# Kernel optimization log

Hardware: AMD Instinct MI355X
Metric: run time of the kernel (lower is better)

## Reference

```python
import jax, jax.numpy as jnp
import numpy as np

B, S, D, E, N = 2, 1024, 1024, 64, 16  # batch, seq, model_dim, embedding_dim, num_splats


def setup_inputs() -> dict:
    key = jax.random.key(0)
    ks = jax.random.split(key, 8)
    inv_sqrt_d = 1.0 / np.sqrt(D)
    return {
        "token_embeddings": jax.random.normal(ks[0], (B, S, D), jnp.float32),
        # position encoder Linear(D, E)
        "pos_W": jax.random.normal(ks[1], (D, E), jnp.float32) * inv_sqrt_d,
        "pos_b": jnp.zeros((E,), jnp.float32),
        "positional_bias": jax.random.normal(ks[2], (1024, E), jnp.float32) * 0.01,
        "splat_positions": jax.random.normal(ks[3], (N, E), jnp.float32) * 0.2,
        "splat_log_scales": jnp.zeros((N,), jnp.float32),
        # q/k/v Linear(D, D, bias=False)
        "q_W": jax.random.normal(ks[4], (D, D), jnp.float32) * inv_sqrt_d,
        "k_W": jax.random.normal(ks[5], (D, D), jnp.float32) * inv_sqrt_d,
        "v_W": jax.random.normal(ks[6], (D, D), jnp.float32) * inv_sqrt_d,
        "splat_gates": jnp.full((N,), 0.5, jnp.float32),
        "residual_weight": jnp.asarray(0.8, jnp.float32),
        "ln_w": jnp.ones((D,), jnp.float32),
        "ln_b": jnp.zeros((D,), jnp.float32),
    }


def reference(token_embeddings, pos_W, pos_b, positional_bias, splat_positions,
              splat_log_scales, q_W, k_W, v_W, splat_gates, residual_weight,
              ln_w, ln_b):
    b, s, d = token_embeddings.shape
    # token positions in splat embedding space: tanh(Linear(x)) + pos_bias[:S]
    positions = jnp.tanh(token_embeddings @ pos_W + pos_b) + positional_bias[:s][None]  # [B,S,E]
    # spatial influence per splat: Gaussian of distance, clamped scales, floor 0.01
    diff = positions[:, :, None, :] - splat_positions[None, None]  # [B,S,N,E]
    dist_sq = jnp.sum(diff * diff, axis=-1)                         # [B,S,N]
    scales = jnp.clip(jnp.exp(splat_log_scales), 0.3, 2.0)
    influence = jnp.maximum(jnp.exp(-0.5 * dist_sq / (scales * scales)), 0.01)  # [B,S,N]

    q = token_embeddings @ q_W
    k = token_embeddings @ k_W
    v = token_embeddings @ v_W

    w = jnp.transpose(influence, (2, 0, 1))      # [N,B,S]
    qw = q[None] * w[..., None]                  # [N,B,S,D]
    kw = k[None] * w[..., None]
    scores = jnp.einsum('nbid,nbjd->nbij', qw, kw) / jnp.sqrt(jnp.asarray(d, jnp.float32))
    causal = jnp.tril(jnp.ones((s, s), bool))
    scores = jnp.where(causal[None, None], scores, -1e9)
    attn = jax.nn.softmax(scores, axis=-1)       # [N,B,S,S]
    out = jnp.einsum('nbij,bjd->nbid', attn, v)  # [N,B,S,D]

    gates = jax.nn.sigmoid(splat_gates)[:, None, None, None]
    combined = jnp.mean(out * gates, axis=0)     # [B,S,D]

    rw = jax.nn.sigmoid(residual_weight)
    o = rw * token_embeddings + (1.0 - rw) * combined
    # LayerNorm (eps=1e-5)
    mu = jnp.mean(o, axis=-1, keepdims=True)
    var = jnp.mean((o - mu) ** 2, axis=-1, keepdims=True)
    return (o - mu) / jnp.sqrt(var + 1e-5) * ln_w + ln_b
```

## Files before the change

### kernel.cpp

```cpp
#include <hip/hip_runtime.h>
#include <hip/hip_bf16.h>
#include <hip/hip_fp16.h>

using bf16 = __hip_bfloat16;
typedef __attribute__((ext_vector_type(8))) short short8;
typedef __attribute__((ext_vector_type(4))) float f32x4;

static constexpr int Bb = 2, Ss = 1024, Dd = 1024, Ee = 64, Nn = 16;

struct Params {
    const float *X, *posW, *posB, *pbias, *spos, *lsc, *qW, *kW, *vW, *gates, *rwp, *lnw, *lnb;
    bf16 *Xb, *Wt, *WpT, *QKV, *Vt, *Aav;
    __half *wh;
    float *qk, *cb, *out;
};

__device__ __forceinline__ unsigned short f2bfr(float f) {
    __hip_bfloat16 h = __float2bfloat16(f);
    return *reinterpret_cast<unsigned short*>(&h);
}

#define GL_LDS(gp, lp) __builtin_amdgcn_global_load_lds( \
    (const __attribute__((address_space(1))) void*)(gp), \
    (__attribute__((address_space(3))) void*)(lp), 16, 0, 0)

__device__ __forceinline__ void do_transpose_f2b(
    const float* __restrict__ in, bf16* __restrict__ out,
    int R, int C, int bx, int by, char* sm)
{
    float (*tile)[65] = (float(*)[65])sm;
    int tx = threadIdx.x & 63, ty = threadIdx.x >> 6;
    int r0 = by * 64, c0 = bx * 64;
    #pragma unroll
    for (int i = 0; i < 16; ++i)
        tile[ty + i*4][tx] = in[(long)(r0 + ty + i*4)*C + c0 + tx];
    __syncthreads();
    #pragma unroll
    for (int i = 0; i < 16; ++i)
        out[(long)(c0 + ty + i*4)*R + r0 + tx] = __float2bfloat16(tile[tx][ty + i*4]);
    __syncthreads();
}

__device__ __forceinline__ void do_gemm6464(
    const bf16* __restrict__ Ab, const bf16* __restrict__ Bw, float* __restrict__ C,
    int Nc, int m0, int n0, int kBeg, int kEnd, float scale, char* sm)
{
    int tid = threadIdx.x, wid = tid >> 6, lane = tid & 63;
    int r16 = lane & 15, quad = lane >> 4;

    f32x4 acc[4];
    #pragma unroll
    for (int j = 0; j < 4; ++j)
        #pragma unroll
        for (int c = 0; c < 4; ++c) acc[j][c] = 0.f;

    const short* Ag = (const short*)Ab;
    const short* Bg = (const short*)Bw;

    int row2[2], kg2[2];
    #pragma unroll
    for (int j = 0; j < 2; ++j) {
        int c = tid + j*256; row2[j] = c >> 3; kg2[j] = (c & 7) ^ (row2[j] & 7);
    }

    auto stage = [&](int k0, int cr) {
        short* sA = (short*)(sm + cr*16384);
        short* sB = (short*)(sm + cr*16384 + 8192);
        #pragma unroll
        for (int j = 0; j < 2; ++j) {
            GL_LDS(Ag + (long)(m0 + row2[j])*1024 + k0 + kg2[j]*8, sA + (tid + j*256)*8);
            GL_LDS(Bg + (long)(n0 + row2[j])*1024 + k0 + kg2[j]*8, sB + (tid + j*256)*8);
        }
    };

    stage(kBeg, 0);
    __syncthreads();
    int cur = 0;
    for (int k0 = kBeg; k0 < kEnd; k0 += 64) {
        if (k0 + 64 < kEnd) stage(k0 + 64, cur ^ 1);
        short* lA = (short*)(sm + cur*16384);
        short* lB = (short*)(sm + cur*16384 + 8192);
        #pragma unroll
        for (int kk = 0; kk < 2; ++kk) {
            int kc = kk*4 + quad;
            int ra = wid*16 + r16;
            short8 af = *(const short8*)(lA + ra*64 + (kc ^ (ra & 7))*8);
            #pragma unroll
            for (int j = 0; j < 4; ++j) {
                int rb = j*16 + r16;
                short8 bfv = *(const short8*)(lB + rb*64 + (kc ^ (rb & 7))*8);
                acc[j] = __builtin_amdgcn_mfma_f32_16x16x32_bf16(af, bfv, acc[j], 0, 0, 0);
            }
        }
        __syncthreads();
        cur ^= 1;
    }

    #pragma unroll
    for (int j = 0; j < 4; ++j)
        #pragma unroll
        for (int rr = 0; rr < 4; ++rr)
            C[(long)(m0 + wid*16 + quad*4 + rr)*Nc + n0 + j*16 + r16] =
                acc[j][rr] * scale;
}

template<int OUT_MODE>
__device__ __forceinline__ void do_gemm128(
    const bf16* __restrict__ Ab, const bf16* __restrict__ Bw, void* __restrict__ Cv,
    int Nc, int m0, int n0, char* sm)
{
    int tid = threadIdx.x, wid = tid >> 6, lane = tid & 63;
    int wm = (wid >> 1) * 64, wnn = (wid & 1) * 64;
    int r16 = lane & 15, quad = lane >> 4;

    f32x4 acc[4][4];
    #pragma unroll
    for (int i = 0; i < 4; ++i)
        #pragma unroll
        for (int j = 0; j < 4; ++j)
            #pragma unroll
            for (int c = 0; c < 4; ++c) acc[i][j][c] = 0.f;

    const short* Ag = (const short*)Ab;
    const short* Bg = (const short*)Bw;

    int rowc[4], kgc[4];
    #pragma unroll
    for (int j = 0; j < 4; ++j) {
        int c = tid + j*256; rowc[j] = c >> 3; kgc[j] = (c & 7) ^ (rowc[j] & 7);
    }

    auto stage = [&](int k0, int cr) {
        short* sA = (short*)(sm + cr*32768);
        short* sB = (short*)(sm + cr*32768 + 16384);
        #pragma unroll
        for (int j = 0; j < 4; ++j)
            GL_LDS(Ag + (long)(m0 + rowc[j])*1024 + k0 + kgc[j]*8, sA + (tid + j*256)*8);
        #pragma unroll
        for (int j = 0; j < 4; ++j)
            GL_LDS(Bg + (long)(n0 + rowc[j])*1024 + k0 + kgc[j]*8, sB + (tid + j*256)*8);
    };

    stage(0, 0);
    __syncthreads();
    int cur = 0;
    for (int k0 = 0; k0 < 1024; k0 += 64) {
        if (k0 + 64 < 1024) stage(k0 + 64, cur ^ 1);
        short* lA = (short*)(sm + cur*32768);
        short* lB = (short*)(sm + cur*32768 + 16384);
        #pragma unroll
        for (int kk = 0; kk < 2; ++kk) {
            int kc = kk*4 + quad;
            short8 af[4], bfv[4];
            #pragma unroll
            for (int i = 0; i < 4; ++i) {
                int r = wm + i*16 + r16;
                af[i] = *(const short8*)(lA + r*64 + (kc ^ (r & 7))*8);
            }
            #pragma unroll
            for (int j = 0; j < 4; ++j) {
                int r = wnn + j*16 + r16;
                bfv[j] = *(const short8*)(lB + r*64 + (kc ^ (r & 7))*8);
            }
            #pragma unroll
            for (int i = 0; i < 4; ++i)
                #pragma unroll
                for (int j = 0; j < 4; ++j)
                    acc[i][j] = __builtin_amdgcn_mfma_f32_16x16x32_bf16(af[i], bfv[j], acc[i][j], 0, 0, 0);
        }
        __syncthreads();
        cur ^= 1;
    }

    if (OUT_MODE == 1) {
        bf16* C = (bf16*)Cv;
        #pragma unroll
        for (int i = 0; i < 4; ++i)
            #pragma unroll
            for (int j = 0; j < 4; ++j)
                #pragma unroll
                for (int rr = 0; rr < 4; ++rr)
                    C[(long)(m0 + wm + i*16 + quad*4 + rr)*Nc + n0 + wnn + j*16 + r16] =
                        __float2bfloat16(acc[i][j][rr]);
    } else {
        __syncthreads();
        bf16 (*lt)[132] = (bf16(*)[132])sm;
        #pragma unroll
        for (int i = 0; i < 4; ++i)
            #pragma unroll
            for (int j = 0; j < 4; ++j)
                #pragma unroll
                for (int rr = 0; rr < 4; ++rr)
                    lt[wnn + j*16 + r16][wm + i*16 + quad*4 + rr] =
                        __float2bfloat16(acc[i][j][rr]);
        __syncthreads();
        bf16* Vb = (bf16*)Cv + (long)(m0 >> 10) * Dd * Ss;
        int s0 = m0 & (Ss - 1);
        int colBase = wid * 32 + (lane >> 4);
        int idx = (lane & 15) * 8;
        #pragma unroll
        for (int it = 0; it < 8; ++it) {
            int col = colBase + it * 4;
            ushort4 v0 = *(const ushort4*)&lt[col][idx];
            ushort4 v1 = *(const ushort4*)&lt[col][idx + 4];
            *(ushort4*)(Vb + (long)(n0 + col)*Ss + s0 + idx)     = v0;
            *(ushort4*)(Vb + (long)(n0 + col)*Ss + s0 + idx + 4) = v1;
        }
    }
}

__device__ __forceinline__ void do_pos(const Params& p, int m0, char* sm)
{
    float (*P)[65]  = (float(*)[65])(sm + 16384);
    float (*sp)[65] = (float(*)[65])(sm + 16384 + 64*65*4);

    int tid = threadIdx.x, wid = tid >> 6, lane = tid & 63;
    int r16 = lane & 15, quad = lane >> 4;

    for (int idx = tid; idx < 16*64; idx += 256)
        sp[idx >> 6][idx & 63] = p.spos[idx];

    f32x4 acc[4];
    #pragma unroll
    for (int j = 0; j < 4; ++j)
        #pragma unroll
        for (int c = 0; c < 4; ++c) acc[j][c] = 0.f;

    int ra = tid >> 2, ka = (tid & 3) * 8;
    const short* Ag = (const short*)p.Xb;
    const short* Bg = (const short*)p.WpT;

    auto stage = [&](int k0, int cr) {
        short* sA = (short*)(sm + cr*8192);
        short* sB = (short*)(sm + cr*8192 + 4096);
        GL_LDS(Ag + (long)(m0+ra)*1024 + k0 + ka, sA + tid*8);
        GL_LDS(Bg + (long)ra*1024 + k0 + ka,      sB + tid*8);
    };

    stage(0, 0);
    __syncthreads();
    int cur = 0;
    for (int k0 = 0; k0 < Dd; k0 += 32) {
        if (k0 + 32 < Dd) stage(k0 + 32, cur ^ 1);
        short* lA = (short*)(sm + cur*8192);
        short* lB = (short*)(sm + cur*8192 + 4096);
        short8 af = *(const short8*)(lA + (wid*16 + r16)*32 + quad*8);
        #pragma unroll
        for (int j = 0; j < 4; ++j) {
            short8 bfv = *(const short8*)(lB + (j*16 + r16)*32 + quad*8);
            acc[j] = __builtin_amdgcn_mfma_f32_16x16x32_bf16(af, bfv, acc[j], 0, 0, 0);
        }
        __syncthreads();
        cur ^= 1;
    }

    #pragma unroll
    for (int j = 0; j < 4; ++j)
        #pragma unroll
        for (int rr = 0; rr < 4; ++rr) {
            int rl  = wid*16 + quad*4 + rr;
            int col = j*16 + r16;
            int srow = (m0 + rl) & (Ss - 1);
            P[rl][col] = tanhf(acc[j][rr] + p.posB[col]) + p.pbias[srow*Ee + col];
        }
    __syncthreads();

    int n  = tid & 15;
    int rb = (tid >> 4) * 4;
    float sc = __expf(p.lsc[n]);
    sc = fminf(fmaxf(sc, 0.3f), 2.0f);
    float inv2 = -0.5f / (sc * sc);
    #pragma unroll
    for (int rr = 0; rr < 4; ++rr) {
        int row = rb + rr;
        float d2 = 0.f;
        #pragma unroll 16
        for (int e = 0; e < 64; ++e) {
            float df = P[row][e] - sp[n][e];
            d2 += df * df;
        }
        float infl = fmaxf(__expf(d2 * inv2), 0.01f);
        p.wh[(long)(m0 + row)*Nn + n] = __float2half(infl);
    }
}

__global__ __launch_bounds__(256) void k_prep(Params p)
{
    __shared__ __align__(16) char sm[64*65*4];
    int z = blockIdx.z;
    if (z < 3) {
        const float* w = (z == 0) ? p.qW : (z == 1) ? p.kW : p.vW;
        do_transpose_f2b(w, p.Wt + (long)z*Dd*Dd, Dd, Dd, blockIdx.x, blockIdx.y, sm);
    } else if (blockIdx.x == 0) {
        do_transpose_f2b(p.posW, p.WpT, Dd, Ee, 0, blockIdx.y, sm);
    } else {
        int job = blockIdx.y * 15 + (blockIdx.x - 1);
        const float4* src = (const float4*)p.X;
        ushort4* dst = (ushort4*)p.Xb;
        for (int idx = job*256 + (int)threadIdx.x; idx < Bb*Ss*Dd/4; idx += 240*256) {
            float4 v = src[idx];
            ushort4 y;
            y.x = f2bfr(v.x); y.y = f2bfr(v.y); y.z = f2bfr(v.z); y.w = f2bfr(v.w);
            dst[idx] = y;
        }
    }
}

__global__ __launch_bounds__(256) void k_qkv_pos(Params p)
{
    __shared__ __align__(16) char sm[65536];
    int job = blockIdx.x;
    if (job < 384) {
        int z = job >> 7, t = job & 127;
        int bm = t >> 3, bn = t & 7;
        if (z < 2)
            do_gemm128<1>(p.Xb, p.Wt + (long)z*Dd*Dd, p.QKV + (long)z*2048*1024,
                          Dd, bm*128, bn*128, sm);
        else
            do_gemm128<2>(p.Xb, p.Wt + (long)2*Dd*Dd, p.Vt,
                          Dd, bm*128, bn*128, sm);
    } else {
        do_pos(p, (job - 384)*64, sm);
    }
}

__global__ __launch_bounds__(256) void k_qkt(Params p)
{
    __shared__ __align__(16) char sm[32768];
    int job = blockIdx.x;
    int b = job / 136, t = job % 136;
    int acc = 0, bm = 0, bn = 0;
    #pragma unroll
    for (int u = 0; u < 16; ++u) {
        int c = u + 1;
        if (t < acc + c) { bm = u; bn = t - acc; break; }
        acc += c;
    }
    const bf16* Qb = p.QKV + (long)b*Ss*Dd;
    const bf16* Kb = p.QKV + (long)2048*1024 + (long)b*Ss*Dd;
    float* dst = p.qk + (long)b*Ss*Ss;
    do_gemm6464(Qb, Kb, dst, Ss, bm*64, bn*64, 0, 1024, 0.03125f, sm);
}

__global__ __launch_bounds__(256) void k_softmax(Params p)
{
    __shared__ __align__(16) char sm[36864 + 256 + 16384];
    __half2 (*wt)[9] = (__half2(*)[9])sm;
    float (*wi4)[16] = (float(*)[16])(sm + 36864);
    float (*qc)[Ss]  = (float(*)[Ss])(sm + 36864 + 256);

    int base = blockIdx.x * 4, b = blockIdx.y;
    int tid = threadIdx.x, wid = tid >> 6, lane = tid & 63;
    int imax = base + 3;

    const __half*  whb  = p.wh + (long)b*Ss*Nn;
    const __half2* whb2 = (const __half2*)whb;

    for (int j = tid; j <= imax; j += 256) {
        #pragma unroll
        for (int h = 0; h < 8; ++h)
            wt[j][h] = whb2[j*8 + h];
    }
    if (tid < 64) wi4[tid >> 4][tid & 15] =
        __half2float(whb[(long)(base + (tid >> 4))*16 + (tid & 15)]);
    __syncthreads();

    int i = base + wid;
    long roff = ((long)b*Ss + i)*Ss;
    const float* q0 = p.qk + roff;
    bf16* arow      = p.Aav + roff;

    float wiR[16], l[16];
    #pragma unroll
    for (int n = 0; n < 16; ++n) { wiR[n] = wi4[wid][n]; l[n] = 0.f; }

    for (int j = lane; j <= i; j += 64) {
        float q = q0[j];
        qc[wid][j] = q;
        #pragma unroll
        for (int h = 0; h < 8; ++h) {
            float2 f = __half22float2(wt[j][h]);
            l[2*h]     += __expf(wiR[2*h]     * f.x * q);
            l[2*h + 1] += __expf(wiR[2*h + 1] * f.y * q);
        }
    }
    #pragma unroll
    for (int n = 0; n < 16; ++n)
        #pragma unroll
        for (int off = 32; off > 0; off >>= 1)
            l[n] += __shfl_xor(l[n], off);

    float coef[16];
    #pragma unroll
    for (int n = 0; n < 16; ++n) {
        float g  = p.gates[n];
        float sg = 1.f / (1.f + __expf(-g));
        coef[n]  = sg / (16.f * l[n]);
    }

    int jLim = (i | 63) + 1;
    for (int j = lane; j < jLim; j += 64) {
        float a = 0.f;
        if (j <= i) {
            float q = qc[wid][j];
            #pragma unroll
            for (int h = 0; h < 8; ++h) {
                float2 f = __half22float2(wt[j][h]);
                a += coef[2*h]     * __expf(wiR[2*h]     * f.x * q);
                a += coef[2*h + 1] * __expf(wiR[2*h + 1] * f.y * q);
            }
        }
        arow[j] = __float2bfloat16(a);
    }
}

__global__ __launch_bounds__(256) void k_av(Params p)
{
    __shared__ __align__(16) char sm[32768];
    int job = blockIdx.x;
    int b  = job >> 8;
    int r  = job & 255;
    int bm = 15 - (r >> 4);
    int bn = r & 15;
    int kEnd = (bm + 1) * 64;

    const bf16* Ab = p.Aav + (long)b*Ss*Ss;
    const bf16* Bw = p.Vt + (long)b*Dd*Ss;
    float* dst = p.cb + (long)b*Ss*Dd;
    do_gemm6464(Ab, Bw, dst, Dd, bm*64, bn*64, 0, kEnd, 1.f, sm);
}

__global__ __launch_bounds__(256) void k_epilogue(Params p)
{
    __shared__ float rs[4], rq[4];
    long row = blockIdx.x;
    int tid = threadIdx.x, wid = tid >> 6, lane = tid & 63;
    float rw = 1.f / (1.f + __expf(-p.rwp[0]));

    float4 c  = ((const float4*)(p.cb + row*Dd))[tid];
    float4 xv = ((const float4*)(p.X + row*Dd))[tid];

    float o[4];
    o[0] = rw * xv.x + (1.f - rw) * c.x;
    o[1] = rw * xv.y + (1.f - rw) * c.y;
    o[2] = rw * xv.z + (1.f - rw) * c.z;
    o[3] = rw * xv.w + (1.f - rw) * c.w;

    float sm1 = o[0] + o[1] + o[2] + o[3];
    float sq  = o[0]*o[0] + o[1]*o[1] + o[2]*o[2] + o[3]*o[3];
    #pragma unroll
    for (int off = 32; off > 0; off >>= 1) { sm1 += __shfl_xor(sm1, off); sq += __shfl_xor(sq, off); }
    if (lane == 0) { rs[wid] = sm1; rq[wid] = sq; }
    __syncthreads();
    sm1 = rs[0] + rs[1] + rs[2] + rs[3];
    sq  = rq[0] + rq[1] + rq[2] + rq[3];
    float mu  = sm1 * (1.f/1024.f);
    float var = sq * (1.f/1024.f) - mu*mu;
    float inv = rsqrtf(var + 1e-5f);

    float4 lw = ((const float4*)p.lnw)[tid];
    float4 lb = ((const float4*)p.lnb)[tid];
    float4 y;
    y.x = (o[0] - mu)*inv*lw.x + lb.x;
    y.y = (o[1] - mu)*inv*lw.y + lb.y;
    y.z = (o[2] - mu)*inv*lw.z + lb.z;
    y.w = (o[3] - mu)*inv*lw.w + lb.w;
    ((float4*)(p.out + row*Dd))[tid] = y;
}

extern "C" void kernel_launch(void* const* d_in, const int* in_sizes, int n_in,
                              void* d_out, int out_size, void* d_ws, size_t ws_size,
                              hipStream_t stream)
{
    Params prm;
    prm.X     = (const float*)d_in[0];
    prm.posW  = (const float*)d_in[1];
    prm.posB  = (const float*)d_in[2];
    prm.pbias = (const float*)d_in[3];
    prm.spos  = (const float*)d_in[4];
    prm.lsc   = (const float*)d_in[5];
    prm.qW    = (const float*)d_in[6];
    prm.kW    = (const float*)d_in[7];
    prm.vW    = (const float*)d_in[8];
    prm.gates = (const float*)d_in[9];
    prm.rwp   = (const float*)d_in[10];
    prm.lnw   = (const float*)d_in[11];
    prm.lnb   = (const float*)d_in[12];

    char* ws = (char*)d_ws;
    size_t off = 0;
    prm.Xb  = (bf16*)(ws + off);   off += (size_t)Bb*Ss*Dd*2;
    prm.Wt  = (bf16*)(ws + off);   off += (size_t)3*Dd*Dd*2;
    prm.WpT = (bf16*)(ws + off);   off += (size_t)Ee*Dd*2;
    prm.QKV = (bf16*)(ws + off);   off += (size_t)2*2048*1024*2;
    prm.Vt  = (bf16*)(ws + off);   off += (size_t)Bb*Dd*Ss*2;
    prm.Aav = (bf16*)(ws + off);   off += (size_t)Bb*Ss*Ss*2;
    prm.wh  = (__half*)(ws + off); off += (size_t)Bb*Ss*Nn*2;
    prm.qk  = (float*)(ws + off);  off += (size_t)Bb*Ss*Ss*4;
    prm.cb  = (float*)(ws + off);  off += (size_t)Bb*Ss*Dd*4;
    prm.out = (float*)d_out;
    (void)ws_size;

    k_prep    <<<dim3(16,16,4), 256, 0, stream>>>(prm);
    k_qkv_pos <<<416,            256, 0, stream>>>(prm);
    k_qkt     <<<272,            256, 0, stream>>>(prm);
    k_softmax <<<dim3(256, 2),   256, 0, stream>>>(prm);
    k_av      <<<512,            256, 0, stream>>>(prm);
    k_epilogue<<<2048,           256, 0, stream>>>(prm);
}
```

Before: 165.2 us.

## Shrink QKV GEMM tiles to 64x128, stage outputs through LDS, reorder pos jobs

The QKV projection GEMM now uses 64x128 tiles instead of 128x128, raising the block count from 384 to 768 so the 256 CUs get a fuller first wave. Output writes now go through LDS and are stored as 16-byte vector rows, replacing scattered 2-byte stores. The position-encoder blocks are moved to the front of the grid so they are scheduled first. Smaller tiles lower data reuse per block and add more global loads of the A operand, plus an extra LDS round trip in the epilogue.

After: 165.1 us. No clear change (-0.0%).

```diff
diff --git a/kernel.cpp b/kernel.cpp
--- a/kernel.cpp
+++ b/kernel.cpp
@@ -104,41 +104,44 @@
                 acc[j][rr] * scale;
 }
 
-template<int OUT_MODE>
-__device__ __forceinline__ void do_gemm128(
+template<int OUT>
+__device__ __forceinline__ void do_gemm64x128(
     const bf16* __restrict__ Ab, const bf16* __restrict__ Bw, void* __restrict__ Cv,
     int Nc, int m0, int n0, char* sm)
 {
     int tid = threadIdx.x, wid = tid >> 6, lane = tid & 63;
-    int wm = (wid >> 1) * 64, wnn = (wid & 1) * 64;
-    int r16 = lane & 15, quad = lane >> 4;
-
-    f32x4 acc[4][4];
+    int wn = wid * 32, r16 = lane & 15, quad = lane >> 4;
+
+    f32x4 acc[4][2];
     #pragma unroll
     for (int i = 0; i < 4; ++i)
         #pragma unroll
-        for (int j = 0; j < 4; ++j)
+        for (int j = 0; j < 2; ++j)
             #pragma unroll
             for (int c = 0; c < 4; ++c) acc[i][j][c] = 0.f;
 
     const short* Ag = (const short*)Ab;
     const short* Bg = (const short*)Bw;
 
-    int rowc[4], kgc[4];
+    int arow[2], akg[2], brow[4], bkg[4];
+    #pragma unroll
+    for (int j = 0; j < 2; ++j) {
+        int c = tid + j*256; arow[j] = c >> 3; akg[j] = (c & 7) ^ (arow[j] & 7);
+    }
     #pragma unroll
     for (int j = 0; j < 4; ++j) {
-        int c = tid + j*256; rowc[j] = c >> 3; kgc[j] = (c & 7) ^ (rowc[j] & 7);
+        int c = tid + j*256; brow[j] = c >> 3; bkg[j] = (c & 7) ^ (brow[j] & 7);
     }
 
     auto stage = [&](int k0, int cr) {
-        short* sA = (short*)(sm + cr*32768);
-        short* sB = (short*)(sm + cr*32768 + 16384);
+        short* sA = (short*)(sm + cr*24576);
+        short* sB = (short*)(sm + cr*24576 + 8192);
+        #pragma unroll
+        for (int j = 0; j < 2; ++j)
+            GL_LDS(Ag + (long)(m0 + arow[j])*1024 + k0 + akg[j]*8, sA + (tid + j*256)*8);
         #pragma unroll
         for (int j = 0; j < 4; ++j)
-            GL_LDS(Ag + (long)(m0 + rowc[j])*1024 + k0 + kgc[j]*8, sA + (tid + j*256)*8);
-        #pragma unroll
-        for (int j = 0; j < 4; ++j)
-            GL_LDS(Bg + (long)(n0 + rowc[j])*1024 + k0 + kgc[j]*8, sB + (tid + j*256)*8);
+            GL_LDS(Bg + (long)(n0 + brow[j])*1024 + k0 + bkg[j]*8, sB + (tid + j*256)*8);
     };
 
     stage(0, 0);
@@ -146,65 +149,66 @@
     int cur = 0;
     for (int k0 = 0; k0 < 1024; k0 += 64) {
         if (k0 + 64 < 1024) stage(k0 + 64, cur ^ 1);
-        short* lA = (short*)(sm + cur*32768);
-        short* lB = (short*)(sm + cur*32768 + 16384);
+        short* lA = (short*)(sm + cur*24576);
+        short* lB = (short*)(sm + cur*24576 + 8192);
         #pragma unroll
         for (int kk = 0; kk < 2; ++kk) {
             int kc = kk*4 + quad;
-            short8 af[4], bfv[4];
+            short8 af[4], bfv[2];
             #pragma unroll
             for (int i = 0; i < 4; ++i) {
-                int r = wm + i*16 + r16;
+                int r = i*16 + r16;
                 af[i] = *(const short8*)(lA + r*64 + (kc ^ (r & 7))*8);
             }
             #pragma unroll
-            for (int j = 0; j < 4; ++j) {
-                int r = wnn + j*16 + r16;
+            for (int j = 0; j < 2; ++j) {
+                int r = wn + j*16 + r16;
                 bfv[j] = *(const short8*)(lB + r*64 + (kc ^ (r & 7))*8);
             }
             #pragma unroll
             for (int i = 0; i < 4; ++i)
                 #pragma unroll
-                for (int j = 0; j < 4; ++j)
+                for (int j = 0; j < 2; ++j)
                     acc[i][j] = __builtin_amdgcn_mfma_f32_16x16x32_bf16(af[i], bfv[j], acc[i][j], 0, 0, 0);
         }
         __syncthreads();
         cur ^= 1;
     }
 
-    if (OUT_MODE == 1) {
-        bf16* C = (bf16*)Cv;
+    if (OUT == 1) {
+        ushort (*lt)[136] = (ushort(*)[136])sm;
         #pragma unroll
         for (int i = 0; i < 4; ++i)
             #pragma unroll
-            for (int j = 0; j < 4; ++j)
+            for (int j = 0; j < 2; ++j)
                 #pragma unroll
                 for (int rr = 0; rr < 4; ++rr)
-                    C[(long)(m0 + wm + i*16 + quad*4 + rr)*Nc + n0 + wnn + j*16 + r16] =
-                        __float2bfloat16(acc[i][j][rr]);
+                    lt[i*16 + quad*4 + rr][wn + j*16 + r16] = f2bfr(acc[i][j][rr]);
+        __syncthreads();
+        ushort* C = (ushort*)Cv;
+        #pragma unroll
+        for (int q = 0; q < 4; ++q) {
+            int c = tid + q*256;
+            int row = c >> 4, off = (c & 15) * 8;
+            *(uint4*)(C + (long)(m0 + row)*Nc + n0 + off) = *(const uint4*)&lt[row][off];
+        }
     } else {
-        __syncthreads();
-        bf16 (*lt)[132] = (bf16(*)[132])sm;
+        ushort (*lt)[72] = (ushort(*)[72])sm;
         #pragma unroll
         for (int i = 0; i < 4; ++i)
             #pragma unroll
-            for (int j = 0; j < 4; ++j)
+            for (int j = 0; j < 2; ++j)
                 #pragma unroll
                 for (int rr = 0; rr < 4; ++rr)
-                    lt[wnn + j*16 + r16][wm + i*16 + quad*4 + rr] =
-                        __float2bfloat16(acc[i][j][rr]);
+                    lt[wn + j*16 + r16][i*16 + quad*4 + rr] = f2bfr(acc[i][j][rr]);
         __syncthreads();
-        bf16* Vb = (bf16*)Cv + (long)(m0 >> 10) * Dd * Ss;
+        ushort* Vb = (ushort*)Cv + (long)(m0 >> 10) * Dd * Ss;
         int s0 = m0 & (Ss - 1);
-        int colBase = wid * 32 + (lane >> 4);
-        int idx = (lane & 15) * 8;
-        #pragma unroll
-        for (int it = 0; it < 8; ++it) {
-            int col = colBase + it * 4;
-            ushort4 v0 = *(const ushort4*)&lt[col][idx];
-            ushort4 v1 = *(const ushort4*)&lt[col][idx + 4];
-            *(ushort4*)(Vb + (long)(n0 + col)*Ss + s0 + idx)     = v0;
-            *(ushort4*)(Vb + (long)(n0 + col)*Ss + s0 + idx + 4) = v1;
+        #pragma unroll
+        for (int q = 0; q < 4; ++q) {
+            int c = tid + q*256;
+            int vrow = c >> 3, off = (c & 7) * 8;
+            *(uint4*)(Vb + (long)(n0 + vrow)*Ss + s0 + off) = *(const uint4*)&lt[vrow][off];
         }
     }
 }
@@ -308,19 +312,21 @@
 
 __global__ __launch_bounds__(256) void k_qkv_pos(Params p)
 {
-    __shared__ __align__(16) char sm[65536];
+    __shared__ __align__(16) char sm[49152];
     int job = blockIdx.x;
-    if (job < 384) {
-        int z = job >> 7, t = job & 127;
-        int bm = t >> 3, bn = t & 7;
-        if (z < 2)
-            do_gemm128<1>(p.Xb, p.Wt + (long)z*Dd*Dd, p.QKV + (long)z*2048*1024,
-                          Dd, bm*128, bn*128, sm);
+    if (job < 32) {
+        do_pos(p, job*64, sm);
+    } else {
+        int t = job - 32;
+        int g = t >> 8;
+        int r = t & 255;
+        int bm = r >> 3, bn = r & 7;
+        if (g < 2)
+            do_gemm64x128<1>(p.Xb, p.Wt + (long)g*Dd*Dd, p.QKV + (long)g*2048*1024,
+                             Dd, bm*64, bn*128, sm);
         else
-            do_gemm128<2>(p.Xb, p.Wt + (long)2*Dd*Dd, p.Vt,
-                          Dd, bm*128, bn*128, sm);
-    } else {
-        do_pos(p, (job - 384)*64, sm);
+            do_gemm64x128<2>(p.Xb, p.Wt + (long)2*Dd*Dd, p.Vt,
+                             Dd, bm*64, bn*128, sm);
     }
 }
 
@@ -502,7 +508,7 @@
     (void)ws_size;
 
     k_prep    <<<dim3(16,16,4), 256, 0, stream>>>(prm);
-    k_qkv_pos <<<416,            256, 0, stream>>>(prm);
+    k_qkv_pos <<<800,            256, 0, stream>>>(prm);
     k_qkt     <<<272,            256, 0, stream>>>(prm);
     k_softmax <<<dim3(256, 2),   256, 0, stream>>>(prm);
     k_av      <<<512,            256, 0, stream>>>(prm);
```
